# Performance work log

Measured on AMD Instinct MI355X. Metric: run time of the kernel, lower is better.

The kernel has to match this reference:

```python
import jax, jax.numpy as jnp
import numpy as np

BS, X_RW, H = 16384, 768, 256  # batch, x + R*W, hidden
D_IN = X_RW + 2 * H            # 1280 = x + R*W + 2*h


def setup_inputs() -> dict:
    key = jax.random.key(0)
    ks = jax.random.split(key, 13)
    scale = 1.0 / np.sqrt(D_IN)  # nn.Linear default init range
    def lin(kw, kb):
        w = jax.random.uniform(kw, (D_IN, H), jnp.float32, -scale, scale)
        b = jax.random.uniform(kb, (H,), jnp.float32, -scale, scale)
        return w, b
    Wi, bi = lin(ks[0], ks[1])
    Wf, bf = lin(ks[2], ks[3])
    Wo, bo = lin(ks[4], ks[5])
    Ws, bs_ = lin(ks[6], ks[7])
    return {
        "input_x": jax.random.normal(ks[8], (BS, X_RW), jnp.float32),
        "previous_time": jax.random.normal(ks[9], (BS, H), jnp.float32),
        "previous_layer": jax.random.normal(ks[10], (BS, H), jnp.float32),
        "old_state": jax.random.normal(ks[11], (BS, H), jnp.float32),
        "Wi": Wi, "bi": bi, "Wf": Wf, "bf": bf,
        "Wo": Wo, "bo": bo, "Ws": Ws, "bs_": bs_,
    }


def reference(input_x, previous_time, previous_layer, old_state,
              Wi, bi, Wf, bf, Wo, bo, Ws, bs_):
    # concat once, fuse the four gate GEMMs into one [D_IN, 4H] GEMM
    s = jnp.concatenate([input_x, previous_time, previous_layer], axis=1)  # [bs, D_IN]
    W4 = jnp.concatenate([Wi, Wf, Wo, Ws], axis=1)   # [D_IN, 4H]
    b4 = jnp.concatenate([bi, bf, bo, bs_], axis=0)  # [4H]
    g = s @ W4 + b4                                   # [bs, 4H]
    i_g, f_g, o_g, c_g = jnp.split(g, 4, axis=1)
    input_gate = jax.nn.sigmoid(i_g)
    forget_gate = jax.nn.sigmoid(f_g)
    output_gate = jax.nn.sigmoid(o_g)
    new_state = forget_gate * old_state + input_gate * jnp.tanh(c_g)
    new_hidden = output_gate * jnp.tanh(new_state)
    return (new_hidden, new_state)
```

## Files before the change

### kernel.cpp

```cpp
#include <hip/hip_runtime.h>
#include <stdint.h>

#define BS   16384
#define XRW  768
#define HD   256
#define DIN  1280
#define N4   1024
#define NKT  20

typedef __attribute__((ext_vector_type(4))) float f32x4;
typedef __attribute__((ext_vector_type(8))) short s16x8;
typedef __attribute__((ext_vector_type(4))) unsigned int u32x4;

__device__ __forceinline__ unsigned short f2bf(float f) {
  uint32_t u = __builtin_bit_cast(uint32_t, f);
  u += 0x7FFFu + ((u >> 16) & 1u);
  return (unsigned short)(u >> 16);
}
__device__ __forceinline__ uint32_t cvtpk(float a, float b) {
  uint32_t d;
  asm("v_cvt_pk_bf16_f32 %0, %1, %2" : "=v"(d) : "v"(a), "v"(b));
  return d;
}
__device__ __forceinline__ float sigmoidf_(float x) {
  return 1.0f / (1.0f + __expf(-x));
}
__device__ __forceinline__ float tanhf_(float x) {
  return 1.0f - 2.0f / (__expf(2.0f * x) + 1.0f);
}
__device__ __forceinline__ void gload16(const void* g, void* l) {
  __builtin_amdgcn_global_load_lds((const __attribute__((address_space(1))) void*)g,
                                   (__attribute__((address_space(3))) void*)l, 16, 0, 0);
}

__global__ void conv_w_kernel(const float* __restrict__ Wi, const float* __restrict__ bi,
                              const float* __restrict__ Wf, const float* __restrict__ bfv,
                              const float* __restrict__ Wo, const float* __restrict__ bo,
                              const float* __restrict__ Ws, const float* __restrict__ bsv,
                              unsigned short* __restrict__ Wt, float* __restrict__ b4) {
  const int np = blockIdx.x;
  const int h = np >> 2, g = np & 3;
  const float* W  = (g == 0) ? Wi : (g == 1) ? Wf : (g == 2) ? Wo : Ws;
  const float* bb = (g == 0) ? bi : (g == 1) ? bfv : (g == 2) ? bo : bsv;
  if (threadIdx.x == 0) b4[np] = bb[h];
  for (int k = threadIdx.x; k < DIN; k += 256)
    Wt[np * DIN + k] = f2bf(W[k * HD + h]);
}

__global__ __launch_bounds__(512, 2)
void lstm_gemm_kernel(const float* __restrict__ X,
                      const float* __restrict__ PT,
                      const float* __restrict__ PL,
                      const unsigned short* __restrict__ Wt,
                      const float* __restrict__ b4,
                      const float* __restrict__ OLD,
                      float* __restrict__ out) {
  __shared__ unsigned char smem[131072];
  const int tid  = threadIdx.x;
  const int wid  = tid >> 6;
  const int lane = tid & 63;

  const int H = blockIdx.x;
  const int xcd = H & 7, slot = H >> 3;
  const int mt = xcd * 8 + (slot >> 2);
  const int nt = slot & 3;
  const int wr = wid >> 2, wc = wid & 3;

  const int r8   = lane >> 3;
  const int scol = ((lane & 7) ^ r8) << 4;
  const char* gB = (const char*)Wt + (size_t)(nt * 256 + wid * 8 + r8) * (DIN * 2) + scol;

#define STAGE_B(t1, o) do {                                                   \
    const int kb_ = (t1) * 128;                                               \
    _Pragma("unroll")                                                         \
    for (int c_ = 0; c_ < 4; ++c_)                                            \
      gload16(gB + (size_t)c_ * (64 * DIN * 2) + kb_,                         \
              &smem[65536 + (o) * 32768 + c_ * 8192 + wid * 1024]);           \
  } while (0)

  const int arow  = tid >> 3;
  const int a7    = tid & 7;
  const int awcol = ((a7 ^ (arow & 7)) << 4);

#define ALOAD(t1, h) do {                                                     \
    const float* asrc_; int astr_, aoff_;                                     \
    if ((t1) < 12)      { asrc_ = X;  astr_ = XRW; aoff_ = (t1) * 64; }       \
    else if ((t1) < 16) { asrc_ = PT; astr_ = HD;  aoff_ = ((t1) - 12) * 64; }\
    else                { asrc_ = PL; astr_ = HD;  aoff_ = ((t1) - 16) * 64; }\
    const float* ga_ = asrc_ + (size_t)(mt * 256 + arow + (h) * 128) * astr_  \
                             + aoff_ + a7 * 8;                                \
    ar0 = *(const f32x4*)(ga_);                                               \
    ar1 = *(const f32x4*)(ga_ + 4);                                           \
    ar2 = *(const f32x4*)(ga_ + (size_t)64 * astr_);                          \
    ar3 = *(const f32x4*)(ga_ + (size_t)64 * astr_ + 4);                      \
  } while (0)

#define AWRITE(o, h) do {                                                     \
    u32x4 w0_, w1_;                                                           \
    w0_.x = cvtpk(ar0.x, ar0.y); w0_.y = cvtpk(ar0.z, ar0.w);                 \
    w0_.z = cvtpk(ar1.x, ar1.y); w0_.w = cvtpk(ar1.z, ar1.w);                 \
    w1_.x = cvtpk(ar2.x, ar2.y); w1_.y = cvtpk(ar2.z, ar2.w);                 \
    w1_.z = cvtpk(ar3.x, ar3.y); w1_.w = cvtpk(ar3.z, ar3.w);                 \
    *(u32x4*)(&smem[(o) * 32768 + ((arow + (h) * 128)      << 7) + awcol]) = w0_; \
    *(u32x4*)(&smem[(o) * 32768 + ((arow + (h) * 128 + 64) << 7) + awcol]) = w1_; \
  } while (0)

  const int rx   = lane & 15;
  const int axor = (lane & 7) << 4;
  const int col0 = (((lane >> 4) << 4)) ^ axor;
  const int col1 = (64 + ((lane >> 4) << 4)) ^ axor;
  const int aRow = (wr * 128 + rx) * 128;
  const int bRow = 65536 + (wc * 64 + rx) * 128;

  f32x4 acc[8][4];
  #pragma unroll
  for (int i = 0; i < 8; ++i)
    #pragma unroll
    for (int j = 0; j < 4; ++j) {
      f32x4 z = {0.0f, 0.0f, 0.0f, 0.0f};
      acc[i][j] = z;
    }

#define VMW(N) asm volatile("s_waitcnt vmcnt(" #N ")" ::: "memory")
#define LGKM0() do { asm volatile("s_waitcnt lgkmcnt(0)" ::: "memory");       \
                     __builtin_amdgcn_sched_barrier(0); } while (0)
#define FRAGS(bo_, kh_col) do {                                               \
    _Pragma("unroll")                                                         \
    for (int mf = 0; mf < 8; ++mf)                                            \
      aq[mf] = *(const s16x8*)(&smem[(bo_) + aRow + mf * 2048 + (kh_col)]);   \
    _Pragma("unroll")                                                         \
    for (int nf = 0; nf < 4; ++nf)                                            \
      bq[nf] = *(const s16x8*)(&smem[(bo_) + bRow + nf * 2048 + (kh_col)]);   \
  } while (0)
#define MFMAS() do {                                                          \
    __builtin_amdgcn_s_setprio(1);                                            \
    _Pragma("unroll")                                                         \
    for (int mf = 0; mf < 8; ++mf)                                            \
      _Pragma("unroll")                                                       \
      for (int nf = 0; nf < 4; ++nf)                                          \
        acc[mf][nf] = __builtin_amdgcn_mfma_f32_16x16x32_bf16(aq[mf], bq[nf], \
                                                      acc[mf][nf], 0, 0, 0);  \
    __builtin_amdgcn_s_setprio(0);                                            \
  } while (0)

  {
    f32x4 ar0, ar1, ar2, ar3;
    ALOAD(0, 0);
    STAGE_B(0, 0);
    VMW(4);
    AWRITE(0, 0);
    ALOAD(0, 1);
    VMW(0);
    AWRITE(0, 1);
    LGKM0();
    __builtin_amdgcn_s_barrier();
  }

  for (int kt = 0; kt < NKT; ++kt) {
    const int c = kt & 1, o = c ^ 1;
    const int bo_ = c << 15;
    const bool pf = (kt + 1) < NKT;
    s16x8 aq[8], bq[4];
    f32x4 ar0, ar1, ar2, ar3;

    if (pf) ALOAD(kt + 1, 0);
    FRAGS(bo_, col0);
    if (pf) STAGE_B(kt + 1, o);
    LGKM0();
    MFMAS();
    VMW(4);
    if (pf) { AWRITE(o, 0); ALOAD(kt + 1, 1); }
    FRAGS(bo_, col1);
    LGKM0();
    MFMAS();
    VMW(0);
    if (pf) AWRITE(o, 1);
    LGKM0();
    __builtin_amdgcn_s_barrier();
  }

  __syncthreads();
  float* creg = (float*)smem + wid * 2048;
  const int mbase = mt * 256 + wr * 128;
  const int hbase = nt * 64 + wc * 16;
  const int bcol  = nt * 256 + wc * 64;
  #pragma unroll
  for (int p = 0; p < 4; ++p) {
    #pragma unroll
    for (int mf2 = 0; mf2 < 2; ++mf2) {
      #pragma unroll
      for (int nf = 0; nf < 4; ++nf) {
        const int lrow = mf2 * 16 + (lane >> 4) * 4;
        const int lcol = nf * 16 + (lane & 15);
        #pragma unroll
        for (int r = 0; r < 4; ++r)
          creg[(lrow + r) * 64 + lcol] = acc[p * 2 + mf2][nf][r];
      }
    }
    #pragma unroll
    for (int j = 0; j < 8; ++j) {
      const int idx = lane + j * 64;
      const int row = idx >> 4;
      const int hc  = idx & 15;
      f32x4 g4 = *(f32x4*)(creg + row * 64 + hc * 4);
      f32x4 bb = *(const f32x4*)(b4 + bcol + hc * 4);
      const int m  = mbase + p * 32 + row;
      const int hg = hbase + hc;
      const float ig = sigmoidf_(g4.x + bb.x);
      const float fg = sigmoidf_(g4.y + bb.y);
      const float og = sigmoidf_(g4.z + bb.z);
      const float cg = tanhf_(g4.w + bb.w);
      const float ns = fg * OLD[m * HD + hg] + ig * cg;
      const float nh = og * tanhf_(ns);
      out[m * HD + hg] = nh;
      out[BS * HD + m * HD + hg] = ns;
    }
  }
#undef STAGE_B
#undef ALOAD
#undef AWRITE
#undef VMW
#undef LGKM0
#undef FRAGS
#undef MFMAS
}

extern "C" void kernel_launch(void* const* d_in, const int* in_sizes, int n_in,
                              void* d_out, int out_size, void* d_ws, size_t ws_size,
                              hipStream_t stream) {
  const float* X   = (const float*)d_in[0];
  const float* PT  = (const float*)d_in[1];
  const float* PL  = (const float*)d_in[2];
  const float* OLD = (const float*)d_in[3];
  const float* Wi  = (const float*)d_in[4];
  const float* bi  = (const float*)d_in[5];
  const float* Wf  = (const float*)d_in[6];
  const float* bfv = (const float*)d_in[7];
  const float* Wo  = (const float*)d_in[8];
  const float* bo  = (const float*)d_in[9];
  const float* Ws  = (const float*)d_in[10];
  const float* bsv = (const float*)d_in[11];
  float* out = (float*)d_out;

  unsigned short* Wt = (unsigned short*)d_ws;
  float*          b4 = (float*)((char*)d_ws + (size_t)N4 * DIN * 2);

  conv_w_kernel<<<N4, 256, 0, stream>>>(Wi, bi, Wf, bfv, Wo, bo, Ws, bsv, Wt, b4);
  lstm_gemm_kernel<<<256, 512, 0, stream>>>(X, PT, PL, Wt, b4, OLD, out);
}
```

Before: 64.10 us.

## Split K-tile main loop into four half-M phases with extra barriers

Result: slower. 70.31 us (+9.7%).

```diff
diff --git a/kernel.cpp b/kernel.cpp
--- a/kernel.cpp
+++ b/kernel.cpp
@@ -70,39 +70,39 @@
   const int scol = ((lane & 7) ^ r8) << 4;
   const char* gB = (const char*)Wt + (size_t)(nt * 256 + wid * 8 + r8) * (DIN * 2) + scol;
 
-#define STAGE_B(t1, o) do {                                                   \
+#define STAGE_B(t1, oB) do {                                                  \
     const int kb_ = (t1) * 128;                                               \
     _Pragma("unroll")                                                         \
     for (int c_ = 0; c_ < 4; ++c_)                                            \
       gload16(gB + (size_t)c_ * (64 * DIN * 2) + kb_,                         \
-              &smem[65536 + (o) * 32768 + c_ * 8192 + wid * 1024]);           \
+              &smem[65536 + (oB) + c_ * 8192 + wid * 1024]);                  \
   } while (0)
 
   const int arow  = tid >> 3;
   const int a7    = tid & 7;
   const int awcol = ((a7 ^ (arow & 7)) << 4);
 
-#define ALOAD(t1, h) do {                                                     \
+#define ALOAD(t1, h, R0, R1, R2, R3) do {                                     \
     const float* asrc_; int astr_, aoff_;                                     \
     if ((t1) < 12)      { asrc_ = X;  astr_ = XRW; aoff_ = (t1) * 64; }       \
     else if ((t1) < 16) { asrc_ = PT; astr_ = HD;  aoff_ = ((t1) - 12) * 64; }\
     else                { asrc_ = PL; astr_ = HD;  aoff_ = ((t1) - 16) * 64; }\
     const float* ga_ = asrc_ + (size_t)(mt * 256 + arow + (h) * 128) * astr_  \
                              + aoff_ + a7 * 8;                                \
-    ar0 = *(const f32x4*)(ga_);                                               \
-    ar1 = *(const f32x4*)(ga_ + 4);                                           \
-    ar2 = *(const f32x4*)(ga_ + (size_t)64 * astr_);                          \
-    ar3 = *(const f32x4*)(ga_ + (size_t)64 * astr_ + 4);                      \
-  } while (0)
-
-#define AWRITE(o, h) do {                                                     \
+    R0 = *(const f32x4*)(ga_);                                                \
+    R1 = *(const f32x4*)(ga_ + 4);                                            \
+    R2 = *(const f32x4*)(ga_ + (size_t)64 * astr_);                           \
+    R3 = *(const f32x4*)(ga_ + (size_t)64 * astr_ + 4);                       \
+  } while (0)
+
+#define AWRITE(oB, h, R0, R1, R2, R3) do {                                    \
     u32x4 w0_, w1_;                                                           \
-    w0_.x = cvtpk(ar0.x, ar0.y); w0_.y = cvtpk(ar0.z, ar0.w);                 \
-    w0_.z = cvtpk(ar1.x, ar1.y); w0_.w = cvtpk(ar1.z, ar1.w);                 \
-    w1_.x = cvtpk(ar2.x, ar2.y); w1_.y = cvtpk(ar2.z, ar2.w);                 \
-    w1_.z = cvtpk(ar3.x, ar3.y); w1_.w = cvtpk(ar3.z, ar3.w);                 \
-    *(u32x4*)(&smem[(o) * 32768 + ((arow + (h) * 128)      << 7) + awcol]) = w0_; \
-    *(u32x4*)(&smem[(o) * 32768 + ((arow + (h) * 128 + 64) << 7) + awcol]) = w1_; \
+    w0_.x = cvtpk(R0.x, R0.y); w0_.y = cvtpk(R0.z, R0.w);                     \
+    w0_.z = cvtpk(R1.x, R1.y); w0_.w = cvtpk(R1.z, R1.w);                     \
+    w1_.x = cvtpk(R2.x, R2.y); w1_.y = cvtpk(R2.z, R2.w);                     \
+    w1_.z = cvtpk(R3.x, R3.y); w1_.w = cvtpk(R3.z, R3.w);                     \
+    *(u32x4*)(&smem[(oB) + ((arow + (h) * 128)      << 7) + awcol]) = w0_;    \
+    *(u32x4*)(&smem[(oB) + ((arow + (h) * 128 + 64) << 7) + awcol]) = w1_;    \
   } while (0)
 
   const int rx   = lane & 15;
@@ -124,59 +124,78 @@
 #define VMW(N) asm volatile("s_waitcnt vmcnt(" #N ")" ::: "memory")
 #define LGKM0() do { asm volatile("s_waitcnt lgkmcnt(0)" ::: "memory");       \
                      __builtin_amdgcn_sched_barrier(0); } while (0)
-#define FRAGS(bo_, kh_col) do {                                               \
-    _Pragma("unroll")                                                         \
-    for (int mf = 0; mf < 8; ++mf)                                            \
-      aq[mf] = *(const s16x8*)(&smem[(bo_) + aRow + mf * 2048 + (kh_col)]);   \
+#define RD_A(bo_, mh, kcol) do {                                              \
+    _Pragma("unroll")                                                         \
+    for (int mf = 0; mf < 4; ++mf)                                            \
+      aq[mf] = *(const s16x8*)(&smem[(bo_) + aRow + ((mh)*4+mf)*2048 + (kcol)]);\
+  } while (0)
+#define RD_B(bo_, kcol) do {                                                  \
     _Pragma("unroll")                                                         \
     for (int nf = 0; nf < 4; ++nf)                                            \
-      bq[nf] = *(const s16x8*)(&smem[(bo_) + bRow + nf * 2048 + (kh_col)]);   \
-  } while (0)
-#define MFMAS() do {                                                          \
+      bq[nf] = *(const s16x8*)(&smem[(bo_) + bRow + nf*2048 + (kcol)]);       \
+  } while (0)
+#define MF16(mh) do {                                                         \
     __builtin_amdgcn_s_setprio(1);                                            \
     _Pragma("unroll")                                                         \
-    for (int mf = 0; mf < 8; ++mf)                                            \
+    for (int mf = 0; mf < 4; ++mf)                                            \
       _Pragma("unroll")                                                       \
       for (int nf = 0; nf < 4; ++nf)                                          \
-        acc[mf][nf] = __builtin_amdgcn_mfma_f32_16x16x32_bf16(aq[mf], bq[nf], \
-                                                      acc[mf][nf], 0, 0, 0);  \
+        acc[(mh)*4+mf][nf] = __builtin_amdgcn_mfma_f32_16x16x32_bf16(         \
+                                 aq[mf], bq[nf], acc[(mh)*4+mf][nf], 0, 0, 0);\
     __builtin_amdgcn_s_setprio(0);                                            \
   } while (0)
 
   {
-    f32x4 ar0, ar1, ar2, ar3;
-    ALOAD(0, 0);
+    f32x4 p0, p1, p2, p3;
+    ALOAD(0, 0, p0, p1, p2, p3);
     STAGE_B(0, 0);
     VMW(4);
-    AWRITE(0, 0);
-    ALOAD(0, 1);
+    AWRITE(0, 0, p0, p1, p2, p3);
+    ALOAD(0, 1, p0, p1, p2, p3);
     VMW(0);
-    AWRITE(0, 1);
+    AWRITE(0, 1, p0, p1, p2, p3);
     LGKM0();
     __builtin_amdgcn_s_barrier();
   }
 
   for (int kt = 0; kt < NKT; ++kt) {
-    const int c = kt & 1, o = c ^ 1;
-    const int bo_ = c << 15;
+    const int bo_ = (kt & 1) << 15;
+    const int oo_ = bo_ ^ 32768;
     const bool pf = (kt + 1) < NKT;
-    s16x8 aq[8], bq[4];
+    s16x8 aq[4], bq[4];
     f32x4 ar0, ar1, ar2, ar3;
-
-    if (pf) ALOAD(kt + 1, 0);
-    FRAGS(bo_, col0);
-    if (pf) STAGE_B(kt + 1, o);
-    LGKM0();
-    MFMAS();
-    VMW(4);
-    if (pf) { AWRITE(o, 0); ALOAD(kt + 1, 1); }
-    FRAGS(bo_, col1);
-    LGKM0();
-    MFMAS();
+    f32x4 as0, as1, as2, as3;
+
+    RD_A(bo_, 0, col0);
+    RD_B(bo_, col0);
+    if (pf) { ALOAD(kt + 1, 0, ar0, ar1, ar2, ar3); STAGE_B(kt + 1, oo_); }
+    __builtin_amdgcn_s_barrier();
+    LGKM0();
+    MF16(0);
+
+    RD_A(bo_, 1, col0);
+    if (pf) ALOAD(kt + 1, 1, as0, as1, as2, as3);
+    __builtin_amdgcn_s_barrier();
+    LGKM0();
+    MF16(1);
+
+    RD_A(bo_, 0, col1);
+    RD_B(bo_, col1);
+    VMW(8);
+    __builtin_amdgcn_sched_barrier(0);
+    if (pf) AWRITE(oo_, 0, ar0, ar1, ar2, ar3);
+    __builtin_amdgcn_s_barrier();
+    LGKM0();
+    MF16(0);
+
+    RD_A(bo_, 1, col1);
     VMW(0);
-    if (pf) AWRITE(o, 1);
-    LGKM0();
-    __builtin_amdgcn_s_barrier();
+    __builtin_amdgcn_sched_barrier(0);
+    if (pf) AWRITE(oo_, 1, as0, as1, as2, as3);
+    LGKM0();
+    __builtin_amdgcn_s_barrier();
+    __builtin_amdgcn_sched_barrier(0);
+    MF16(1);
   }
 
   __syncthreads();
@@ -221,8 +240,9 @@
 #undef AWRITE
 #undef VMW
 #undef LGKM0
-#undef FRAGS
-#undef MFMAS
+#undef RD_A
+#undef RD_B
+#undef MF16
 }
 
 extern "C" void kernel_launch(void* const* d_in, const int* in_sizes, int n_in,
```

## Reorder weight columns so each lane holds all four gates, drop LDS epilogue

Applied to the files above, without the earlier changes.

Result: no change. 63.12 us (-1.5%).

```diff
diff --git a/kernel.cpp b/kernel.cpp
--- a/kernel.cpp
+++ b/kernel.cpp
@@ -33,16 +33,15 @@
                                    (__attribute__((address_space(3))) void*)l, 16, 0, 0);
 }
 
-__global__ void conv_w_kernel(const float* __restrict__ Wi, const float* __restrict__ bi,
-                              const float* __restrict__ Wf, const float* __restrict__ bfv,
-                              const float* __restrict__ Wo, const float* __restrict__ bo,
-                              const float* __restrict__ Ws, const float* __restrict__ bsv,
-                              unsigned short* __restrict__ Wt, float* __restrict__ b4) {
+__global__ void conv_w_kernel(const float* __restrict__ Wi,
+                              const float* __restrict__ Wf,
+                              const float* __restrict__ Wo,
+                              const float* __restrict__ Ws,
+                              unsigned short* __restrict__ Wt) {
   const int np = blockIdx.x;
-  const int h = np >> 2, g = np & 3;
-  const float* W  = (g == 0) ? Wi : (g == 1) ? Wf : (g == 2) ? Wo : Ws;
-  const float* bb = (g == 0) ? bi : (g == 1) ? bfv : (g == 2) ? bo : bsv;
-  if (threadIdx.x == 0) b4[np] = bb[h];
+  const int g = (np >> 4) & 3;
+  const int h = ((np >> 6) << 4) + (np & 15);
+  const float* W = (g == 0) ? Wi : (g == 1) ? Wf : (g == 2) ? Wo : Ws;
   for (int k = threadIdx.x; k < DIN; k += 256)
     Wt[np * DIN + k] = f2bf(W[k * HD + h]);
 }
@@ -52,7 +51,10 @@
                       const float* __restrict__ PT,
                       const float* __restrict__ PL,
                       const unsigned short* __restrict__ Wt,
-                      const float* __restrict__ b4,
+                      const float* __restrict__ BI,
+                      const float* __restrict__ BF,
+                      const float* __restrict__ BO,
+                      const float* __restrict__ BSv,
                       const float* __restrict__ OLD,
                       float* __restrict__ out) {
   __shared__ unsigned char smem[131072];
@@ -70,39 +72,39 @@
   const int scol = ((lane & 7) ^ r8) << 4;
   const char* gB = (const char*)Wt + (size_t)(nt * 256 + wid * 8 + r8) * (DIN * 2) + scol;
 
-#define STAGE_B(t1, o) do {                                                   \
+#define STAGE_B(t1, oB) do {                                                  \
     const int kb_ = (t1) * 128;                                               \
     _Pragma("unroll")                                                         \
     for (int c_ = 0; c_ < 4; ++c_)                                            \
       gload16(gB + (size_t)c_ * (64 * DIN * 2) + kb_,                         \
-              &smem[65536 + (o) * 32768 + c_ * 8192 + wid * 1024]);           \
+              &smem[65536 + (oB) + c_ * 8192 + wid * 1024]);                  \
   } while (0)
 
   const int arow  = tid >> 3;
   const int a7    = tid & 7;
   const int awcol = ((a7 ^ (arow & 7)) << 4);
 
-#define ALOAD(t1, h) do {                                                     \
+#define ALOAD(t1, h, R0, R1, R2, R3) do {                                     \
     const float* asrc_; int astr_, aoff_;                                     \
     if ((t1) < 12)      { asrc_ = X;  astr_ = XRW; aoff_ = (t1) * 64; }       \
     else if ((t1) < 16) { asrc_ = PT; astr_ = HD;  aoff_ = ((t1) - 12) * 64; }\
     else                { asrc_ = PL; astr_ = HD;  aoff_ = ((t1) - 16) * 64; }\
     const float* ga_ = asrc_ + (size_t)(mt * 256 + arow + (h) * 128) * astr_  \
                              + aoff_ + a7 * 8;                                \
-    ar0 = *(const f32x4*)(ga_);                                               \
-    ar1 = *(const f32x4*)(ga_ + 4);                                           \
-    ar2 = *(const f32x4*)(ga_ + (size_t)64 * astr_);                          \
-    ar3 = *(const f32x4*)(ga_ + (size_t)64 * astr_ + 4);                      \
-  } while (0)
-
-#define AWRITE(o, h) do {                                                     \
+    R0 = *(const f32x4*)(ga_);                                                \
+    R1 = *(const f32x4*)(ga_ + 4);                                            \
+    R2 = *(const f32x4*)(ga_ + (size_t)64 * astr_);                           \
+    R3 = *(const f32x4*)(ga_ + (size_t)64 * astr_ + 4);                       \
+  } while (0)
+
+#define AWRITE(oB, h, R0, R1, R2, R3) do {                                    \
     u32x4 w0_, w1_;                                                           \
-    w0_.x = cvtpk(ar0.x, ar0.y); w0_.y = cvtpk(ar0.z, ar0.w);                 \
-    w0_.z = cvtpk(ar1.x, ar1.y); w0_.w = cvtpk(ar1.z, ar1.w);                 \
-    w1_.x = cvtpk(ar2.x, ar2.y); w1_.y = cvtpk(ar2.z, ar2.w);                 \
-    w1_.z = cvtpk(ar3.x, ar3.y); w1_.w = cvtpk(ar3.z, ar3.w);                 \
-    *(u32x4*)(&smem[(o) * 32768 + ((arow + (h) * 128)      << 7) + awcol]) = w0_; \
-    *(u32x4*)(&smem[(o) * 32768 + ((arow + (h) * 128 + 64) << 7) + awcol]) = w1_; \
+    w0_.x = cvtpk(R0.x, R0.y); w0_.y = cvtpk(R0.z, R0.w);                     \
+    w0_.z = cvtpk(R1.x, R1.y); w0_.w = cvtpk(R1.z, R1.w);                     \
+    w1_.x = cvtpk(R2.x, R2.y); w1_.y = cvtpk(R2.z, R2.w);                     \
+    w1_.z = cvtpk(R3.x, R3.y); w1_.w = cvtpk(R3.z, R3.w);                     \
+    *(u32x4*)(&smem[(oB) + ((arow + (h) * 128)      << 7) + awcol]) = w0_;    \
+    *(u32x4*)(&smem[(oB) + ((arow + (h) * 128 + 64) << 7) + awcol]) = w1_;    \
   } while (0)
 
   const int rx   = lane & 15;
@@ -144,14 +146,14 @@
   } while (0)
 
   {
-    f32x4 ar0, ar1, ar2, ar3;
-    ALOAD(0, 0);
+    f32x4 p0, p1, p2, p3;
+    ALOAD(0, 0, p0, p1, p2, p3);
     STAGE_B(0, 0);
     VMW(4);
-    AWRITE(0, 0);
-    ALOAD(0, 1);
+    AWRITE(0, 0, p0, p1, p2, p3);
+    ALOAD(0, 1, p0, p1, p2, p3);
     VMW(0);
-    AWRITE(0, 1);
+    AWRITE(0, 1, p0, p1, p2, p3);
     LGKM0();
     __builtin_amdgcn_s_barrier();
   }
@@ -159,61 +161,50 @@
   for (int kt = 0; kt < NKT; ++kt) {
     const int c = kt & 1, o = c ^ 1;
     const int bo_ = c << 15;
+    const int oo_ = o << 15;
     const bool pf = (kt + 1) < NKT;
     s16x8 aq[8], bq[4];
     f32x4 ar0, ar1, ar2, ar3;
 
-    if (pf) ALOAD(kt + 1, 0);
+    if (pf) ALOAD(kt + 1, 0, ar0, ar1, ar2, ar3);
     FRAGS(bo_, col0);
-    if (pf) STAGE_B(kt + 1, o);
+    if (pf) STAGE_B(kt + 1, oo_);
     LGKM0();
     MFMAS();
     VMW(4);
-    if (pf) { AWRITE(o, 0); ALOAD(kt + 1, 1); }
+    if (pf) { AWRITE(oo_, 0, ar0, ar1, ar2, ar3); ALOAD(kt + 1, 1, ar0, ar1, ar2, ar3); }
     FRAGS(bo_, col1);
     LGKM0();
     MFMAS();
     VMW(0);
-    if (pf) AWRITE(o, 1);
+    if (pf) AWRITE(oo_, 1, ar0, ar1, ar2, ar3);
     LGKM0();
     __builtin_amdgcn_s_barrier();
   }
 
-  __syncthreads();
-  float* creg = (float*)smem + wid * 2048;
-  const int mbase = mt * 256 + wr * 128;
-  const int hbase = nt * 64 + wc * 16;
-  const int bcol  = nt * 256 + wc * 64;
-  #pragma unroll
-  for (int p = 0; p < 4; ++p) {
+  {
+    const int hq = nt * 64 + wc * 16 + rx;
+    const float bbi = BI[hq], bbf = BF[hq], bbo = BO[hq], bbs = BSv[hq];
+    const int m0 = mt * 256 + wr * 128 + (lane >> 4) * 4;
+    float* outNS = out + (size_t)BS * HD;
     #pragma unroll
-    for (int mf2 = 0; mf2 < 2; ++mf2) {
+    for (int mf = 0; mf < 8; ++mf) {
+      const int mrow = m0 + mf * 16;
+      float old_[4];
       #pragma unroll
-      for (int nf = 0; nf < 4; ++nf) {
-        const int lrow = mf2 * 16 + (lane >> 4) * 4;
-        const int lcol = nf * 16 + (lane & 15);
-        #pragma unroll
-        for (int r = 0; r < 4; ++r)
-          creg[(lrow + r) * 64 + lcol] = acc[p * 2 + mf2][nf][r];
+      for (int r = 0; r < 4; ++r)
+        old_[r] = OLD[(size_t)(mrow + r) * HD + hq];
+      #pragma unroll
+      for (int r = 0; r < 4; ++r) {
+        const float ig = sigmoidf_(acc[mf][0][r] + bbi);
+        const float fg = sigmoidf_(acc[mf][1][r] + bbf);
+        const float og = sigmoidf_(acc[mf][2][r] + bbo);
+        const float cg = tanhf_(acc[mf][3][r] + bbs);
+        const float ns = fg * old_[r] + ig * cg;
+        const float nh = og * tanhf_(ns);
+        out[(size_t)(mrow + r) * HD + hq]   = nh;
+        outNS[(size_t)(mrow + r) * HD + hq] = ns;
       }
-    }
-    #pragma unroll
-    for (int j = 0; j < 8; ++j) {
-      const int idx = lane + j * 64;
-      const int row = idx >> 4;
-      const int hc  = idx & 15;
-      f32x4 g4 = *(f32x4*)(creg + row * 64 + hc * 4);
-      f32x4 bb = *(const f32x4*)(b4 + bcol + hc * 4);
-      const int m  = mbase + p * 32 + row;
-      const int hg = hbase + hc;
-      const float ig = sigmoidf_(g4.x + bb.x);
-      const float fg = sigmoidf_(g4.y + bb.y);
-      const float og = sigmoidf_(g4.z + bb.z);
-      const float cg = tanhf_(g4.w + bb.w);
-      const float ns = fg * OLD[m * HD + hg] + ig * cg;
-      const float nh = og * tanhf_(ns);
-      out[m * HD + hg] = nh;
-      out[BS * HD + m * HD + hg] = ns;
     }
   }
 #undef STAGE_B
@@ -243,8 +234,7 @@
   float* out = (float*)d_out;
 
   unsigned short* Wt = (unsigned short*)d_ws;
-  float*          b4 = (float*)((char*)d_ws + (size_t)N4 * DIN * 2);
-
-  conv_w_kernel<<<N4, 256, 0, stream>>>(Wi, bi, Wf, bfv, Wo, bo, Ws, bsv, Wt, b4);
-  lstm_gemm_kernel<<<256, 512, 0, stream>>>(X, PT, PL, Wt, b4, OLD, out);
-}
+
+  conv_w_kernel<<<N4, 256, 0, stream>>>(Wi, Wf, Wo, Ws, Wt);
+  lstm_gemm_kernel<<<256, 512, 0, stream>>>(X, PT, PL, Wt, bi, bfv, bo, bsv, OLD, out);
+}
```
